# Kernel tuning notes

Hardware: AMD Instinct MI355X
Metric: run time of the kernel (lower is better)

## Reference

```python
import jax, jax.numpy as jnp
import numpy as np

NUM_HEADS = 12


def setup_inputs() -> dict:
    key = jax.random.key(0)
    k1, k2, k3, k4 = jax.random.split(key, 4)
    B, N, C = 8, 1024, 768
    x = jax.random.normal(k1, (B, N, C), dtype=jnp.float32)
    w_qkv = jax.random.normal(k2, (3 * C, C), dtype=jnp.float32) * 0.02
    w_proj = jax.random.normal(k3, (C, C), dtype=jnp.float32) * 0.02
    b_proj = jax.random.normal(k4, (C,), dtype=jnp.float32) * 0.02
    return {"x": x, "w_qkv": w_qkv, "w_proj": w_proj, "b_proj": b_proj}


def reference(x, w_qkv, w_proj, b_proj):
    B, N, C = x.shape
    H = NUM_HEADS
    D = C // H
    scale = D ** -0.5
    # qkv projection (HMQLinear with quant=False is a plain linear, bias=False)
    qkv = jnp.einsum('bnc,oc->bno', x, w_qkv)          # [B,N,3C]
    qkv = qkv.reshape(B, N, 3, H, D).transpose(2, 0, 3, 1, 4)  # [3,B,H,N,D]
    q, k, v = qkv[0], qkv[1], qkv[2]
    # HMQMulQK (passthrough matmul), scale applied after QK^T as in source
    attn = jnp.einsum('bhqd,bhkd->bhqk', q, k) * scale  # [B,H,N,N]
    attn = jax.nn.softmax(attn, axis=-1)                # HMQSoftmax
    out = jnp.einsum('bhqk,bhkd->bhqd', attn, v)        # HMQMulSV
    out = out.transpose(0, 2, 1, 3).reshape(B, N, C)
    # output projection (HMQLinear, default bias=True)
    return jnp.einsum('bnc,oc->bno', out, w_proj) + b_proj
```

## Files before the change

### kernel.cpp

```cpp
#include <hip/hip_runtime.h>
#include <hip/hip_bf16.h>
#include <stdint.h>

typedef __attribute__((ext_vector_type(8))) short short8;
typedef __attribute__((ext_vector_type(4))) float f32x4;
typedef __attribute__((ext_vector_type(16))) float f32x16;
typedef __attribute__((ext_vector_type(4))) unsigned short us4;

#define AS1 __attribute__((address_space(1)))
#define AS3 __attribute__((address_space(3)))

__device__ inline unsigned short f2bf(float f) {
    unsigned int u = __float_as_uint(f);
    u += 0x7FFFu + ((u >> 16) & 1u);
    return (unsigned short)(u >> 16);
}

__device__ inline unsigned int cvtpk(float lo, float hi) {
    unsigned int r;
    asm("v_cvt_pk_bf16_f32 %0, %1, %2" : "=v"(r) : "v"(lo), "v"(hi));
    return r;
}

__device__ inline void pl32swap(unsigned int& a, unsigned int& b) {
    asm volatile("v_permlane32_swap_b32 %0, %1" : "+v"(a), "+v"(b));
}

__device__ inline float fexp2(float x) {
#if __has_builtin(__builtin_amdgcn_exp2f)
    return __builtin_amdgcn_exp2f(x);
#else
    return exp2f(x);
#endif
}

#define VMW(N) asm volatile("s_waitcnt vmcnt(" #N ")" ::: "memory")
#define BARR() __builtin_amdgcn_s_barrier()

__global__ void cvt_all(const float* __restrict__ x, const float* __restrict__ wq,
                        const float* __restrict__ wp,
                        unsigned short* __restrict__ xb,
                        unsigned short* __restrict__ wqb,
                        unsigned short* __restrict__ wpb) {
    const int X4 = 1572864, Q4 = 442368;
    int i = blockIdx.x * blockDim.x + threadIdx.x;
    const float* src; unsigned short* dst; int j;
    if (i < X4) { src = x; dst = xb; j = i; }
    else if (i < X4 + Q4) { src = wq; dst = wqb; j = i - X4; }
    else { src = wp; dst = wpb; j = i - X4 - Q4; }
    float4 v = ((const float4*)src)[j];
    us4 o;
    o.x = f2bf(v.x); o.y = f2bf(v.y); o.z = f2bf(v.z); o.w = f2bf(v.w);
    ((us4*)dst)[j] = o;
}

#define BM 128
#define BN 128

template<int MODE>
__global__ __launch_bounds__(256)
void gemm_bt(const unsigned short* __restrict__ A,
             const unsigned short* __restrict__ Bm,
             unsigned short* __restrict__ Qo, unsigned short* __restrict__ Ko,
             unsigned short* __restrict__ Vto,
             float* __restrict__ Co, const float* __restrict__ bias,
             int M, int N, int K)
{
    __shared__ __align__(16) unsigned short As[3][BM * 32];
    __shared__ __align__(16) unsigned short Bs[3][BM * 32];
    const int tid = threadIdx.x;
    const int wave = tid >> 6, lane = tid & 63;
    const int tr = blockIdx.x * BM;
    const int tc = blockIdx.y * BN;
    const int wm = wave >> 1, wn = wave & 1;

    f32x4 acc[4][4] = {};

    auto stage = [&](int it, int buf) {
#pragma unroll
        for (int i = 0; i < 2; ++i) {
            int cid = i * 256 + tid;
            int r = cid >> 2, cd = cid & 3;
            int sc = cd ^ (r & 3);
            __builtin_amdgcn_global_load_lds(
                (const AS1 void*)(A + (size_t)(tr + r) * K + it * 32 + sc * 8),
                (AS3 void*)(&As[buf][(i * 256 + wave * 64) * 8]), 16, 0, 0);
            __builtin_amdgcn_global_load_lds(
                (const AS1 void*)(Bm + (size_t)(tc + r) * K + it * 32 + sc * 8),
                (AS3 void*)(&Bs[buf][(i * 256 + wave * 64) * 8]), 16, 0, 0);
        }
    };

    const int nIt = K / 32;
    stage(0, 0);
    stage(1, 1);
    int cb = 0, sb = 2;

    for (int it = 0; it < nIt; ++it) {
        if (it + 1 < nIt) { VMW(4); }
        else              { VMW(0); }
        BARR();
        if (it + 2 < nIt) stage(it + 2, sb);

        short8 af[4], bfr[4];
#pragma unroll
        for (int mt = 0; mt < 4; ++mt) {
            int rr = wm * 64 + mt * 16 + (lane & 15);
            af[mt] = *(const short8*)&As[cb][rr * 32 + (((lane >> 4) ^ (rr & 3)) * 8)];
        }
#pragma unroll
        for (int nt = 0; nt < 4; ++nt) {
            int rr = wn * 64 + nt * 16 + (lane & 15);
            bfr[nt] = *(const short8*)&Bs[cb][rr * 32 + (((lane >> 4) ^ (rr & 3)) * 8)];
        }
#pragma unroll
        for (int mt = 0; mt < 4; ++mt)
#pragma unroll
            for (int nt = 0; nt < 4; ++nt)
                acc[mt][nt] = __builtin_amdgcn_mfma_f32_16x16x32_bf16(af[mt], bfr[nt], acc[mt][nt], 0, 0, 0);

        cb = (cb == 2) ? 0 : cb + 1;
        sb = (sb == 2) ? 0 : sb + 1;
    }

    const float QSCALE = 0.18033688011112042f;
#pragma unroll
    for (int mt = 0; mt < 4; ++mt) {
#pragma unroll
        for (int nt = 0; nt < 4; ++nt) {
            int col = tc + wn * 64 + nt * 16 + (lane & 15);
            int row0 = tr + wm * 64 + mt * 16 + (lane >> 4) * 4;
            if constexpr (MODE == 0) {
                int s = (col >= 1536) ? 2 : (col >= 768 ? 1 : 0);
                int rem = col - s * 768;
                int h = rem >> 6, d = rem & 63;
                int b = row0 >> 10, n0 = row0 & 1023;
                int bh = b * 12 + h;
                if (s == 2) {
                    us4 pv;
#pragma unroll
                    for (int r = 0; r < 4; ++r) pv[r] = f2bf(acc[mt][nt][r]);
                    int qd = (n0 >> 2) & 3;
                    int nst = n0 + ((qd == 1) ? 4 : (qd == 2) ? -4 : 0);
                    *(us4*)&Vto[((size_t)bh * 64 + d) * 1024 + nst] = pv;
                } else {
                    unsigned short* dst = (s == 0) ? Qo : Ko;
                    float sc = (s == 0) ? QSCALE : 1.0f;
#pragma unroll
                    for (int r = 0; r < 4; ++r)
                        dst[((size_t)bh * 1024 + n0 + r) * 64 + d] = f2bf(acc[mt][nt][r] * sc);
                }
            } else {
#pragma unroll
                for (int r = 0; r < 4; ++r)
                    Co[(size_t)(row0 + r) * N + col] = acc[mt][nt][r] + bias[col];
            }
        }
    }
}

__global__ __launch_bounds__(256, 3)
void attn_kernel(const unsigned short* __restrict__ Q,
                 const unsigned short* __restrict__ Kg,
                 const unsigned short* __restrict__ Vt,
                 unsigned short* __restrict__ Og)
{
    __shared__ __align__(16) unsigned short KV[3][2][64 * 64];

    const int tid = threadIdx.x;
    const int wave = tid >> 6, lane = tid & 63;
    const int l31 = lane & 31, hi = lane >> 5;

    const int id = blockIdx.x;
    const int swz = (id & 7) * 96 + (id >> 3);
    const int bh = swz >> 3, qb = swz & 7;

    const int b = bh / 12, h = bh % 12;
    const size_t baseK = (size_t)bh * 1024 * 64;
    const size_t baseV = (size_t)bh * 64 * 1024;
    const int q0 = qb * 128 + wave * 32;

    short8 qf[4];
#pragma unroll
    for (int ds = 0; ds < 4; ++ds)
        qf[ds] = *(const short8*)&Q[baseK + (size_t)(q0 + l31) * 64 + ds * 16 + hi * 8];

    f32x16 ot0 = {}, ot1 = {};
    float l = 0.f;

    auto stage = [&](int kt, int buf) {
        const unsigned short* gK = Kg + baseK + (size_t)kt * 64 * 64;
        const unsigned short* gV = Vt + baseV + kt * 64;
#pragma unroll
        for (int i = 0; i < 2; ++i) {
            int c = wave * 128 + i * 64 + lane;
            int r = c >> 3, cc = c & 7;
            int sw = (cc ^ (r & 7)) * 8;
            __builtin_amdgcn_global_load_lds(
                (const AS1 void*)(gK + r * 64 + sw),
                (AS3 void*)(&KV[buf][0][(wave * 128 + i * 64) * 8]), 16, 0, 0);
            __builtin_amdgcn_global_load_lds(
                (const AS1 void*)(gV + (size_t)r * 1024 + sw),
                (AS3 void*)(&KV[buf][1][(wave * 128 + i * 64) * 8]), 16, 0, 0);
        }
    };

    auto rfrag = [&](const unsigned short* s, int row, int cc) -> short8 {
        return *(const short8*)&s[(row * 8 + (cc ^ (row & 7))) * 8];
    };

    auto pack8 = [&](const f32x16& S, int r0) -> short8 {
        union { unsigned int u[4]; short8 s; } fr;
#pragma unroll
        for (int w = 0; w < 4; ++w)
            fr.u[w] = cvtpk(S[r0 + 2 * w], S[r0 + 2 * w + 1]);
        return fr.s;
    };

    stage(0, 0);
    stage(1, 1);
    int cb = 0, sb = 2;

    for (int kt = 0; kt < 16; ++kt) {
        if (kt < 15) { VMW(4); }
        else         { VMW(0); }
        BARR();
        if (kt < 14) stage(kt + 2, sb);

        f32x16 st0 = {}, st1 = {};
        __builtin_amdgcn_s_setprio(1);
#pragma unroll
        for (int ds = 0; ds < 4; ++ds) {
            short8 k0 = rfrag(KV[cb][0], l31, ds * 2 + hi);
            short8 k1 = rfrag(KV[cb][0], 32 + l31, ds * 2 + hi);
            st0 = __builtin_amdgcn_mfma_f32_32x32x16_bf16(k0, qf[ds], st0, 0, 0, 0);
            st1 = __builtin_amdgcn_mfma_f32_32x32x16_bf16(k1, qf[ds], st1, 0, 0, 0);
        }
        __builtin_amdgcn_s_setprio(0);

        short8 v00 = rfrag(KV[cb][1], l31, 0 + hi);
        short8 v10 = rfrag(KV[cb][1], 32 + l31, 0 + hi);
        short8 v01 = rfrag(KV[cb][1], l31, 2 + hi);
        short8 v11 = rfrag(KV[cb][1], 32 + l31, 2 + hi);

#pragma unroll
        for (int i = 0; i < 16; ++i) st0[i] = fexp2(st0[i]);
        short8 paf0 = pack8(st0, 0);
        short8 paf1 = pack8(st0, 8);

        __builtin_amdgcn_s_setprio(1);
        ot0 = __builtin_amdgcn_mfma_f32_32x32x16_bf16(v00, paf0, ot0, 0, 0, 0);
        ot1 = __builtin_amdgcn_mfma_f32_32x32x16_bf16(v10, paf0, ot1, 0, 0, 0);
        ot0 = __builtin_amdgcn_mfma_f32_32x32x16_bf16(v01, paf1, ot0, 0, 0, 0);
        ot1 = __builtin_amdgcn_mfma_f32_32x32x16_bf16(v11, paf1, ot1, 0, 0, 0);
        __builtin_amdgcn_s_setprio(0);

        short8 v02 = rfrag(KV[cb][1], l31, 4 + hi);
        short8 v12 = rfrag(KV[cb][1], 32 + l31, 4 + hi);
        short8 v03 = rfrag(KV[cb][1], l31, 6 + hi);
        short8 v13 = rfrag(KV[cb][1], 32 + l31, 6 + hi);
#pragma unroll
        for (int i = 0; i < 16; ++i) st1[i] = fexp2(st1[i]);
        short8 paf2 = pack8(st1, 0);
        short8 paf3 = pack8(st1, 8);

        __builtin_amdgcn_s_setprio(1);
        ot0 = __builtin_amdgcn_mfma_f32_32x32x16_bf16(v02, paf2, ot0, 0, 0, 0);
        ot1 = __builtin_amdgcn_mfma_f32_32x32x16_bf16(v12, paf2, ot1, 0, 0, 0);
        ot0 = __builtin_amdgcn_mfma_f32_32x32x16_bf16(v03, paf3, ot0, 0, 0, 0);
        ot1 = __builtin_amdgcn_mfma_f32_32x32x16_bf16(v13, paf3, ot1, 0, 0, 0);
        __builtin_amdgcn_s_setprio(0);

        float su[8];
#pragma unroll
        for (int i = 0; i < 8; ++i)
            su[i] = (st0[2 * i] + st0[2 * i + 1]) + (st1[2 * i] + st1[2 * i + 1]);
#pragma unroll
        for (int s = 4; s > 0; s >>= 1)
#pragma unroll
            for (int i = 0; i < 4; ++i)
                if (i < s) su[i] += su[i + s];
        l += su[0];

        cb = (cb == 2) ? 0 : cb + 1;
        sb = (sb == 2) ? 0 : sb + 1;
    }

    {
        unsigned int pu = __float_as_uint(l), pv = pu;
        pl32swap(pu, pv);
        l += __uint_as_float(hi ? pv : pu);
    }

    float inv = 1.f / l;
#pragma unroll
    for (int i = 0; i < 16; ++i) { ot0[i] *= inv; ot1[i] *= inv; }

    BARR();

    unsigned int* ow = (unsigned int*)(&KV[0][0][0]) + wave * 1152;
#pragma unroll
    for (int dt = 0; dt < 2; ++dt)
#pragma unroll
        for (int rp = 0; rp < 8; ++rp) {
            unsigned int w = (dt == 0) ? cvtpk(ot0[2 * rp], ot0[2 * rp + 1])
                                       : cvtpk(ot1[2 * rp], ot1[2 * rp + 1]);
            int wd = dt * 16 + 4 * (rp >> 1) + 2 * hi + (rp & 1);
            ow[l31 * 36 + wd] = w;
        }
#pragma unroll
    for (int i = 0; i < 4; ++i) {
        int c = i * 64 + lane;
        int qr = c >> 3, ch = c & 7;
        short8 vv = *(const short8*)((const unsigned short*)&ow[qr * 36 + ch * 4]);
        *(short8*)&Og[(size_t)(b * 1024 + q0 + qr) * 768 + h * 64 + ch * 8] = vv;
    }
}

extern "C" void kernel_launch(void* const* d_in, const int* in_sizes, int n_in,
                              void* d_out, int out_size, void* d_ws, size_t ws_size,
                              hipStream_t stream) {
    const float* x      = (const float*)d_in[0];
    const float* w_qkv  = (const float*)d_in[1];
    const float* w_proj = (const float*)d_in[2];
    const float* b_proj = (const float*)d_in[3];
    float* out = (float*)d_out;

    const int Bb = 8, Nn = 1024, C = 768;
    const int M = Bb * Nn;
    const size_t XB = (size_t)M * C;
    const size_t WQ = (size_t)3 * C * C;
    const size_t WP = (size_t)C * C;
    const size_t QE = (size_t)96 * 1024 * 64;

    unsigned short* xb  = (unsigned short*)d_ws;
    unsigned short* wqb = xb + XB;
    unsigned short* wpb = wqb + WQ;
    unsigned short* Qb  = wpb + WP;
    unsigned short* Kb  = Qb + QE;
    unsigned short* Vtb = Kb + QE;
    unsigned short* AO  = Vtb + QE;

    cvt_all<<<8448, 256, 0, stream>>>(x, w_qkv, w_proj, xb, wqb, wpb);

    gemm_bt<0><<<dim3(M / BM, (3 * C) / BN), 256, 0, stream>>>(
        xb, wqb, Qb, Kb, Vtb, nullptr, nullptr, M, 3 * C, C);

    attn_kernel<<<768, 256, 0, stream>>>(Qb, Kb, Vtb, AO);

    gemm_bt<1><<<dim3(M / BM, C / BN), 256, 0, stream>>>(
        AO, wpb, nullptr, nullptr, nullptr, out, b_proj, M, C, C);
}
```

Before: 114.8 us.

## Load GEMM B operand directly into registers, double-buffer A in LDS

The B operand is now read straight from global memory into per-lane registers at MFMA fragment layout, and no longer staged through LDS. The A operand's LDS staging drops from triple to double buffering with a two-step unrolled loop. This cuts LDS traffic and shared memory footprint, which may allow more resident blocks. In exchange every wave issues its own uncoalesced-ish 16-byte global loads for B, and the loop now waits for all outstanding loads (VMW(0)) each step, so there is less latency hiding.

```diff
diff --git a/kernel.cpp b/kernel.cpp
--- a/kernel.cpp
+++ b/kernel.cpp
@@ -66,8 +66,7 @@
              float* __restrict__ Co, const float* __restrict__ bias,
              int M, int N, int K)
 {
-    __shared__ __align__(16) unsigned short As[3][BM * 32];
-    __shared__ __align__(16) unsigned short Bs[3][BM * 32];
+    __shared__ __align__(16) unsigned short As[2][BM * 32];
     const int tid = threadIdx.x;
     const int wave = tid >> 6, lane = tid & 63;
     const int tr = blockIdx.x * BM;
@@ -76,7 +75,12 @@
 
     f32x4 acc[4][4] = {};
 
-    auto stage = [&](int it, int buf) {
+    const unsigned short* Brow[4];
+#pragma unroll
+    for (int nt = 0; nt < 4; ++nt)
+        Brow[nt] = Bm + (size_t)(tc + wn * 64 + nt * 16 + (lane & 15)) * K + ((lane >> 4) * 8);
+
+    auto stageA = [&](int it, int buf) {
 #pragma unroll
         for (int i = 0; i < 2; ++i) {
             int cid = i * 256 + tid;
@@ -85,42 +89,39 @@
             __builtin_amdgcn_global_load_lds(
                 (const AS1 void*)(A + (size_t)(tr + r) * K + it * 32 + sc * 8),
                 (AS3 void*)(&As[buf][(i * 256 + wave * 64) * 8]), 16, 0, 0);
-            __builtin_amdgcn_global_load_lds(
-                (const AS1 void*)(Bm + (size_t)(tc + r) * K + it * 32 + sc * 8),
-                (AS3 void*)(&Bs[buf][(i * 256 + wave * 64) * 8]), 16, 0, 0);
-        }
-    };
-
-    const int nIt = K / 32;
-    stage(0, 0);
-    stage(1, 1);
-    int cb = 0, sb = 2;
-
-    for (int it = 0; it < nIt; ++it) {
-        if (it + 1 < nIt) { VMW(4); }
-        else              { VMW(0); }
-        BARR();
-        if (it + 2 < nIt) stage(it + 2, sb);
-
-        short8 af[4], bfr[4];
+        }
+    };
+    auto loadB = [&](int it, short8* set) {
+#pragma unroll
+        for (int nt = 0; nt < 4; ++nt)
+            set[nt] = *(const short8*)(Brow[nt] + it * 32);
+    };
+    auto comp = [&](int buf, const short8* set) {
+        short8 af[4];
 #pragma unroll
         for (int mt = 0; mt < 4; ++mt) {
             int rr = wm * 64 + mt * 16 + (lane & 15);
-            af[mt] = *(const short8*)&As[cb][rr * 32 + (((lane >> 4) ^ (rr & 3)) * 8)];
-        }
-#pragma unroll
-        for (int nt = 0; nt < 4; ++nt) {
-            int rr = wn * 64 + nt * 16 + (lane & 15);
-            bfr[nt] = *(const short8*)&Bs[cb][rr * 32 + (((lane >> 4) ^ (rr & 3)) * 8)];
+            af[mt] = *(const short8*)&As[buf][rr * 32 + (((lane >> 4) ^ (rr & 3)) * 8)];
         }
 #pragma unroll
         for (int mt = 0; mt < 4; ++mt)
 #pragma unroll
             for (int nt = 0; nt < 4; ++nt)
-                acc[mt][nt] = __builtin_amdgcn_mfma_f32_16x16x32_bf16(af[mt], bfr[nt], acc[mt][nt], 0, 0, 0);
-
-        cb = (cb == 2) ? 0 : cb + 1;
-        sb = (sb == 2) ? 0 : sb + 1;
+                acc[mt][nt] = __builtin_amdgcn_mfma_f32_16x16x32_bf16(af[mt], set[nt], acc[mt][nt], 0, 0, 0);
+    };
+
+    const int nIt = K / 32;
+    short8 bA[4], bB[4];
+    stageA(0, 0);
+    loadB(0, bA);
+
+    for (int j = 0; j < nIt; j += 2) {
+        VMW(0); BARR();
+        if (j + 1 < nIt) { stageA(j + 1, 1); loadB(j + 1, bB); }
+        comp(0, bA);
+        VMW(0); BARR();
+        if (j + 2 < nIt) { stageA(j + 2, 0); loadB(j + 2, bA); }
+        comp(1, bB);
     }
 
     const float QSCALE = 0.18033688011112042f;
```

Result: slower. 155.1 us (+35.2%).
